# Performance work log

Hardware: AMD Instinct MI355X
Metric: run time of the kernel (lower is better)

Reference implementation:

```python
import jax, jax.numpy as jnp
import numpy as np

NUM_USERS = 600000
NUM_ITEMS = 400000
NUM_NODES = NUM_USERS + NUM_ITEMS
DIM = 64
NUM_EDGES = 8000000


def setup_inputs() -> dict:
    key = jax.random.key(0)
    k1, k2, k3, k4 = jax.random.split(key, 4)
    users_emb = jax.random.normal(k1, (NUM_USERS, DIM), dtype=jnp.float32)
    items_emb = jax.random.normal(k2, (NUM_ITEMS, DIM), dtype=jnp.float32)
    edge_index = jax.random.randint(k3, (2, NUM_EDGES), 0, NUM_NODES, dtype=jnp.int64)
    edge_values = jax.random.uniform(k4, (NUM_EDGES,), dtype=jnp.float32)
    return {
        "users_emb": users_emb,
        "items_emb": items_emb,
        "edge_index": edge_index,
        "edge_values": edge_values,
    }


def reference(users_emb, items_emb, edge_index, edge_values):
    # all_emb = cat([users_emb, items_emb])  -> [N, d]
    num_user = users_emb.shape[0]
    num_item = items_emb.shape[0]
    all_emb = jnp.concatenate([users_emb, items_emb], axis=0)
    # SpMM: out[r] = sum_{e: row[e]==r} val[e] * all_emb[col[e]]
    rows, cols = edge_index[0], edge_index[1]
    messages = all_emb[cols] * edge_values[:, None]  # [E, d] gather + scale
    out = jax.ops.segment_sum(messages, rows, num_segments=num_user + num_item)
    h_u2 = out[:num_user]
    h_i2 = out[num_user:]
    return (h_u2, h_i2)
```

## Files before the change

kernel.cpp:

```cpp
#include <hip/hip_runtime.h>

#define DIM 64
#define RPB 1024
#define RPB_SHIFT 10
#define NBMAX 1024
#define CHUNK 6144
#define EPT 24
#define CAPT 36
#define NPG 4
#define NPB 128
#define REC_CAP 1536

typedef unsigned long long u64;
typedef unsigned int u32;
typedef unsigned short u16;
typedef float f4v __attribute__((ext_vector_type(4)));
typedef _Float16 h4 __attribute__((ext_vector_type(4)));
typedef _Float16 h8 __attribute__((ext_vector_type(8)));

__global__ void detect_idx_width(const unsigned int* __restrict__ idx_words,
                                 int* __restrict__ flag) {
    __shared__ unsigned int s_or[256];
    unsigned int acc = 0;
    for (int i = threadIdx.x; i < 4096; i += blockDim.x)
        acc |= idx_words[2 * i + 1];
    s_or[threadIdx.x] = acc;
    __syncthreads();
    for (int s = 128; s > 0; s >>= 1) {
        if (threadIdx.x < s) s_or[threadIdx.x] |= s_or[threadIdx.x + s];
        __syncthreads();
    }
    if (threadIdx.x == 0) *flag = (s_or[0] == 0) ? 1 : 0;
}

__device__ __forceinline__ int load_idx(const void* ei, int use64, long long i) {
    return use64 ? (int)((const long long*)ei)[i] : ((const int*)ei)[i];
}

__device__ __forceinline__ int load_idx_nt(const void* ei, int use64, long long i) {
    return use64 ? (int)__builtin_nontemporal_load(&((const long long*)ei)[i])
                 : __builtin_nontemporal_load(&((const int*)ei)[i]);
}

__device__ __forceinline__ u32 quad_scan_ex(u32 qs, u32* wtot, int tid, u32* total_out) {
    u32 inc = qs;
    #pragma unroll
    for (int d = 1; d < 64; d <<= 1) {
        u32 v = __shfl_up(inc, d, 64);
        if ((tid & 63) >= d) inc += v;
    }
    if ((tid & 63) == 63) wtot[tid >> 6] = inc;
    __syncthreads();
    int w = tid >> 6;
    u32 woff = 0;
    #pragma unroll
    for (int k = 0; k < 3; ++k) woff += (k < w) ? wtot[k] : 0;
    if (total_out) *total_out = wtot[0] + wtot[1] + wtot[2] + wtot[3];
    return woff + inc - qs;
}

__global__ __launch_bounds__(256) void convert_emb(const f4v* __restrict__ u4,
                                                   const f4v* __restrict__ i4,
                                                   long long usz4, long long tot4,
                                                   h4* __restrict__ dst) {
    long long stride = (long long)gridDim.x * blockDim.x;
    for (long long idx = (long long)blockIdx.x * blockDim.x + threadIdx.x;
         idx < tot4; idx += stride) {
        const f4v* src = (idx < usz4) ? (u4 + idx) : (i4 + (idx - usz4));
        f4v f = __builtin_nontemporal_load(src);
        h4 o;
        o.x = (_Float16)f.x; o.y = (_Float16)f.y;
        o.z = (_Float16)f.z; o.w = (_Float16)f.w;
        dst[idx] = o;
    }
}

__global__ __launch_bounds__(256) void hist_coarse(const void* __restrict__ ei,
                                                   const int* __restrict__ flag,
                                                   int* __restrict__ counts,
                                                   int num_edges) {
    __shared__ int h[NBMAX];
    for (int b = threadIdx.x; b < NBMAX; b += 256) h[b] = 0;
    __syncthreads();
    int use64 = *flag;
    long long tid = (long long)blockIdx.x * 256 + threadIdx.x;
    long long stride = (long long)gridDim.x * 256;
    long long npairs = (long long)num_edges >> 1;
    const u64* p = (const u64*)ei;
    if (use64) {
        for (long long e = tid; e < npairs; e += stride) {
            u64 a = __builtin_nontemporal_load(&p[2 * e]);
            u64 b = __builtin_nontemporal_load(&p[2 * e + 1]);
            atomicAdd(&h[(int)(u32)a >> RPB_SHIFT], 1);
            atomicAdd(&h[(int)(u32)b >> RPB_SHIFT], 1);
        }
    } else {
        for (long long e = tid; e < npairs; e += stride) {
            u64 v = __builtin_nontemporal_load(&p[e]);
            atomicAdd(&h[(int)(u32)v >> RPB_SHIFT], 1);
            atomicAdd(&h[(int)(u32)(v >> 32) >> RPB_SHIFT], 1);
        }
    }
    if (tid == 0 && (num_edges & 1)) {
        int r = load_idx(ei, use64, num_edges - 1);
        atomicAdd(&h[r >> RPB_SHIFT], 1);
    }
    __syncthreads();
    for (int b = threadIdx.x; b < NBMAX; b += 256)
        if (h[b]) atomicAdd(&counts[b], h[b]);
}

__global__ __launch_bounds__(256) void scan_buckets(const int* __restrict__ counts,
                                                    int* __restrict__ offs,
                                                    int* __restrict__ gcursor,
                                                    int* __restrict__ offs2, int nbkt) {
    __shared__ u32 wtot[4];
    int t = threadIdx.x;
    int4 h = ((const int4*)counts)[t];
    u32 qs = (u32)(h.x + h.y + h.z + h.w);
    u32 total;
    u32 ex = quad_scan_ex(qs, wtot, t, &total);
    int o0 = (int)ex, o1 = o0 + h.x, o2 = o1 + h.y, o3 = o2 + h.z;
    offs[4*t] = o0; offs[4*t+1] = o1; offs[4*t+2] = o2; offs[4*t+3] = o3;
    gcursor[4*t] = o0; gcursor[4*t+1] = o1; gcursor[4*t+2] = o2; gcursor[4*t+3] = o3;
    if (t == 255) {
        offs[NBMAX] = (int)total;
        offs2[(long long)nbkt << RPB_SHIFT] = (int)total;
    }
}

__global__ __launch_bounds__(256, 2) void bin_edges(const void* __restrict__ ei,
                                                    const float* __restrict__ vals,
                                                    const int* __restrict__ flag,
                                                    int* __restrict__ gcursor,
                                                    u64* __restrict__ recs,
                                                    int num_edges) {
    __shared__ u32 hist[NBMAX];
    __shared__ u32 scanL[NBMAX];
    __shared__ u32 gbase[NBMAX];
    __shared__ u32 wtot[4];
    __shared__ u64 payload[CHUNK];
    __shared__ u16 bidv[CHUNK];

    int tid = threadIdx.x;
    long long base = (long long)blockIdx.x * CHUNK;
    int n = (int)min((long long)CHUNK, (long long)num_edges - base);
    int use64 = *flag;

    for (int b = tid; b < NBMAX; b += 256) hist[b] = 0;
    __syncthreads();

    int rows_[EPT]; int cols_[EPT]; float ws_[EPT];
    #pragma unroll
    for (int i = 0; i < EPT; ++i) {
        int j = tid + i * 256;
        rows_[i] = -1;
        if (j < n) {
            long long e = base + j;
            rows_[i] = load_idx_nt(ei, use64, e);
            cols_[i] = load_idx_nt(ei, use64, (long long)num_edges + e);
            ws_[i]   = __builtin_nontemporal_load(&vals[e]);
            atomicAdd(&hist[rows_[i] >> RPB_SHIFT], 1u);
        }
    }
    __syncthreads();

    u32 h0 = hist[4*tid], h1 = hist[4*tid+1], h2 = hist[4*tid+2], h3 = hist[4*tid+3];
    u32 ex = quad_scan_ex(h0 + h1 + h2 + h3, wtot, tid, nullptr);
    scanL[4*tid]   = ex;
    scanL[4*tid+1] = ex + h0;
    scanL[4*tid+2] = ex + h0 + h1;
    scanL[4*tid+3] = ex + h0 + h1 + h2;
    __syncthreads();

    for (int b = tid; b < NBMAX; b += 256) {
        u32 c = hist[b];
        gbase[b] = c ? (u32)atomicAdd(&gcursor[b], (int)c) : 0u;
    }
    __syncthreads();
    for (int b = tid; b < NBMAX; b += 256) hist[b] = scanL[b];
    __syncthreads();

    #pragma unroll
    for (int i = 0; i < EPT; ++i) {
        if (rows_[i] >= 0) {
            int b = rows_[i] >> RPB_SHIFT;
            u32 pos = atomicAdd(&hist[b], 1u);
            u32 rl = (u32)(rows_[i] & (RPB - 1));
            payload[pos] = ((u64)__float_as_uint(ws_[i]) << 32) | (rl << 20) | (u32)cols_[i];
            bidv[pos] = (u16)b;
        }
    }
    __syncthreads();

    for (int j = tid; j < n; j += 256) {
        u64 rec = payload[j];
        int b = bidv[j];
        recs[gbase[b] + (u32)j - scanL[b]] = rec;
    }
}

__global__ __launch_bounds__(256, 2) void sort_bucket(const int* __restrict__ offs,
                                                      u64* __restrict__ recs,
                                                      int* __restrict__ offs2) {
    __shared__ u32 bins[RPB];
    __shared__ u32 wtot[4];
    int b = blockIdx.x;
    int t = threadIdx.x;
    int beg = offs[b], end = offs[b + 1];
    int cnt = end - beg;
    int row0 = b << RPB_SHIFT;

    if (cnt > CAPT * 256) {
        for (int i = t; i < RPB; i += 256) offs2[row0 + i] = -(b + 1);
        return;
    }

    u64 r_[CAPT];
    #pragma unroll
    for (int k = 0; k < CAPT; ++k) {
        int j = t + k * 256;
        r_[k] = (j < cnt) ? recs[beg + j] : 0ull;
    }
    for (int i = t; i < RPB; i += 256) bins[i] = 0;
    __syncthreads();

    #pragma unroll
    for (int k = 0; k < CAPT; ++k) {
        int j = t + k * 256;
        if (j < cnt) atomicAdd(&bins[(u32)(r_[k] >> 20) & (RPB - 1)], 1u);
    }
    __syncthreads();

    u32 c0[4]; u32 s = 0;
    #pragma unroll
    for (int i = 0; i < 4; ++i) { c0[i] = bins[t * 4 + i]; s += c0[i]; }
    u32 ex = quad_scan_ex(s, wtot, t, nullptr);
    #pragma unroll
    for (int i = 0; i < 4; ++i) {
        bins[t * 4 + i] = ex;
        offs2[row0 + t * 4 + i] = beg + (int)ex;
        ex += c0[i];
    }
    __syncthreads();

    #pragma unroll
    for (int k = 0; k < CAPT; ++k) {
        int j = t + k * 256;
        if (j < cnt) {
            u32 rl = (u32)(r_[k] >> 20) & (RPB - 1);
            u32 pos = atomicAdd(&bins[rl], 1u);
            recs[beg + pos] = r_[k];
        }
    }
}

#define ACC8(P0, P1, W, V) \
    P0.x += W * (float)V[0]; P0.y += W * (float)V[1]; \
    P0.z += W * (float)V[2]; P0.w += W * (float)V[3]; \
    P1.x += W * (float)V[4]; P1.y += W * (float)V[5]; \
    P1.z += W * (float)V[6]; P1.w += W * (float)V[7];

__global__ __launch_bounds__(256) void gather_nodes_h(const int* __restrict__ offs,
                                                      const int* __restrict__ offs2,
                                                      const u64* __restrict__ recs,
                                                      const h8* __restrict__ hemb8,
                                                      float* __restrict__ out,
                                                      int num_nodes) {
    __shared__ int s_offs[NPB + 1];
    __shared__ int s_bad;
    __shared__ u64 s_recs[REC_CAP];

    int tid = threadIdx.x;
    int l8  = tid & 7;
    int g   = tid >> 3;
    long long n0 = (long long)blockIdx.x * NPB;

    if (tid == 0) s_bad = 0;
    __syncthreads();
    if (tid <= NPB) {
        int v = offs2[n0 + tid];
        s_offs[tid] = v;
        if (v < 0) s_bad = 1;
    }
    __syncthreads();

    int rbeg = s_offs[0];
    int cnt  = s_offs[NPB] - rbeg;
    bool fast = (s_bad == 0) && ((u32)cnt <= (u32)REC_CAP);

    if (fast) {
        for (int j = tid; j < cnt; j += 256)
            s_recs[j] = __builtin_nontemporal_load(&recs[rbeg + j]);
    }
    __syncthreads();

    if (fast) {
        for (int nn = 0; nn < NPG; ++nn) {
            int ln = g * NPG + nn;
            int node = (int)n0 + ln;
            if (node >= num_nodes) break;
            int beg = s_offs[ln] - rbeg;
            int end = s_offs[ln + 1] - rbeg;

            float4 p0 = make_float4(0.f,0.f,0.f,0.f), p1 = make_float4(0.f,0.f,0.f,0.f);
            float4 q0 = make_float4(0.f,0.f,0.f,0.f), q1 = make_float4(0.f,0.f,0.f,0.f);

            int i = beg;
            for (; i + 8 <= end; i += 8) {
                u64 s0 = s_recs[i];     u64 s1 = s_recs[i + 1];
                u64 s2 = s_recs[i + 2]; u64 s3 = s_recs[i + 3];
                u64 s4 = s_recs[i + 4]; u64 s5 = s_recs[i + 5];
                u64 s6 = s_recs[i + 6]; u64 s7 = s_recs[i + 7];
                h8 v0 = hemb8[(((u32)s0 & 0xFFFFFu) << 3) + l8];
                h8 v1 = hemb8[(((u32)s1 & 0xFFFFFu) << 3) + l8];
                h8 v2 = hemb8[(((u32)s2 & 0xFFFFFu) << 3) + l8];
                h8 v3 = hemb8[(((u32)s3 & 0xFFFFFu) << 3) + l8];
                h8 v4 = hemb8[(((u32)s4 & 0xFFFFFu) << 3) + l8];
                h8 v5 = hemb8[(((u32)s5 & 0xFFFFFu) << 3) + l8];
                h8 v6 = hemb8[(((u32)s6 & 0xFFFFFu) << 3) + l8];
                h8 v7 = hemb8[(((u32)s7 & 0xFFFFFu) << 3) + l8];
                float w0 = __uint_as_float((u32)(s0 >> 32));
                float w1 = __uint_as_float((u32)(s1 >> 32));
                float w2 = __uint_as_float((u32)(s2 >> 32));
                float w3 = __uint_as_float((u32)(s3 >> 32));
                float w4 = __uint_as_float((u32)(s4 >> 32));
                float w5 = __uint_as_float((u32)(s5 >> 32));
                float w6 = __uint_as_float((u32)(s6 >> 32));
                float w7 = __uint_as_float((u32)(s7 >> 32));
                ACC8(p0, p1, w0, v0); ACC8(q0, q1, w1, v1);
                ACC8(p0, p1, w2, v2); ACC8(q0, q1, w3, v3);
                ACC8(p0, p1, w4, v4); ACC8(q0, q1, w5, v5);
                ACC8(p0, p1, w6, v6); ACC8(q0, q1, w7, v7);
            }
            if (i < end) {
                int last = end - 1;
                int e1 = min(i + 1, last), e2 = min(i + 2, last);
                int e3 = min(i + 3, last), e4 = min(i + 4, last);
                int e5 = min(i + 5, last), e6 = min(i + 6, last);
                u64 s0 = s_recs[i];  u64 s1 = s_recs[e1];
                u64 s2 = s_recs[e2]; u64 s3 = s_recs[e3];
                u64 s4 = s_recs[e4]; u64 s5 = s_recs[e5];
                u64 s6 = s_recs[e6];
                h8 v0 = hemb8[(((u32)s0 & 0xFFFFFu) << 3) + l8];
                h8 v1 = hemb8[(((u32)s1 & 0xFFFFFu) << 3) + l8];
                h8 v2 = hemb8[(((u32)s2 & 0xFFFFFu) << 3) + l8];
                h8 v3 = hemb8[(((u32)s3 & 0xFFFFFu) << 3) + l8];
                h8 v4 = hemb8[(((u32)s4 & 0xFFFFFu) << 3) + l8];
                h8 v5 = hemb8[(((u32)s5 & 0xFFFFFu) << 3) + l8];
                h8 v6 = hemb8[(((u32)s6 & 0xFFFFFu) << 3) + l8];
                float w0 = __uint_as_float((u32)(s0 >> 32));
                float w1 = (i + 1 < end) ? __uint_as_float((u32)(s1 >> 32)) : 0.f;
                float w2 = (i + 2 < end) ? __uint_as_float((u32)(s2 >> 32)) : 0.f;
                float w3 = (i + 3 < end) ? __uint_as_float((u32)(s3 >> 32)) : 0.f;
                float w4 = (i + 4 < end) ? __uint_as_float((u32)(s4 >> 32)) : 0.f;
                float w5 = (i + 5 < end) ? __uint_as_float((u32)(s5 >> 32)) : 0.f;
                float w6 = (i + 6 < end) ? __uint_as_float((u32)(s6 >> 32)) : 0.f;
                ACC8(p0, p1, w0, v0); ACC8(q0, q1, w1, v1);
                ACC8(p0, p1, w2, v2); ACC8(q0, q1, w3, v3);
                ACC8(p0, p1, w4, v4); ACC8(q0, q1, w5, v5);
                ACC8(p0, p1, w6, v6);
            }

            p0.x += q0.x; p0.y += q0.y; p0.z += q0.z; p0.w += q0.w;
            p1.x += q1.x; p1.y += q1.y; p1.z += q1.z; p1.w += q1.w;
            f4v o0; o0.x = p0.x; o0.y = p0.y; o0.z = p0.z; o0.w = p0.w;
            f4v o1; o1.x = p1.x; o1.y = p1.y; o1.z = p1.z; o1.w = p1.w;
            f4v* dst = (f4v*)out + ((long long)node << 4) + (l8 << 1);
            __builtin_nontemporal_store(o0, dst);
            __builtin_nontemporal_store(o1, dst + 1);
        }
    } else {
        for (int nn = 0; nn < NPG; ++nn) {
            int ln = g * NPG + nn;
            int node = (int)n0 + ln;
            if (node >= num_nodes) break;
            int beg = s_offs[ln];
            int end = s_offs[ln + 1];
            if (beg < 0) { int b = node >> RPB_SHIFT; beg = offs[b]; end = offs[b + 1]; }
            else if (end < 0) { end = offs[(node >> RPB_SHIFT) + 1]; }
            u32 rl = (u32)(node & (RPB - 1));

            float4 p0 = make_float4(0.f,0.f,0.f,0.f), p1 = make_float4(0.f,0.f,0.f,0.f);
            float4 q0 = make_float4(0.f,0.f,0.f,0.f), q1 = make_float4(0.f,0.f,0.f,0.f);
            int last = end - 1;
            u32 rm = RPB - 1;
            for (int i = beg; i < end; i += 4) {
                int e1 = min(i + 1, last), e2 = min(i + 2, last), e3 = min(i + 3, last);
                u64 s0 = recs[i];  u64 s1 = recs[e1];
                u64 s2 = recs[e2]; u64 s3 = recs[e3];
                h8 v0 = hemb8[(((u32)s0 & 0xFFFFFu) << 3) + l8];
                h8 v1 = hemb8[(((u32)s1 & 0xFFFFFu) << 3) + l8];
                h8 v2 = hemb8[(((u32)s2 & 0xFFFFFu) << 3) + l8];
                h8 v3 = hemb8[(((u32)s3 & 0xFFFFFu) << 3) + l8];
                float w0 = ((((u32)(s0 >> 20)) & rm) == rl)
                           ? __uint_as_float((u32)(s0 >> 32)) : 0.f;
                float w1 = (((((u32)(s1 >> 20)) & rm) == rl) & (i + 1 < end))
                           ? __uint_as_float((u32)(s1 >> 32)) : 0.f;
                float w2 = (((((u32)(s2 >> 20)) & rm) == rl) & (i + 2 < end))
                           ? __uint_as_float((u32)(s2 >> 32)) : 0.f;
                float w3 = (((((u32)(s3 >> 20)) & rm) == rl) & (i + 3 < end))
                           ? __uint_as_float((u32)(s3 >> 32)) : 0.f;
                ACC8(p0, p1, w0, v0); ACC8(q0, q1, w1, v1);
                ACC8(p0, p1, w2, v2); ACC8(q0, q1, w3, v3);
            }
            p0.x += q0.x; p0.y += q0.y; p0.z += q0.z; p0.w += q0.w;
            p1.x += q1.x; p1.y += q1.y; p1.z += q1.z; p1.w += q1.w;
            f4v o0; o0.x = p0.x; o0.y = p0.y; o0.z = p0.z; o0.w = p0.w;
            f4v o1; o1.x = p1.x; o1.y = p1.y; o1.z = p1.z; o1.w = p1.w;
            f4v* dst = (f4v*)out + ((long long)node << 4) + (l8 << 1);
            __builtin_nontemporal_store(o0, dst);
            __builtin_nontemporal_store(o1, dst + 1);
        }
    }
}

__device__ __forceinline__ void gstep(u64 s, u32 rl,
                                      const float* __restrict__ users,
                                      const float* __restrict__ items_m,
                                      int num_users, int l16, float4& a) {
    int c = (int)(s & 0xFFFFFu);
    float w = __uint_as_float((u32)(s >> 32));
    w = (((u32)(s >> 20) & (RPB - 1)) == rl) ? w : 0.f;
    const float* p = ((c < num_users) ? users : items_m) + ((u32)c << 6);
    float4 m = reinterpret_cast<const float4*>(p)[l16];
    a.x += w * m.x; a.y += w * m.y; a.z += w * m.z; a.w += w * m.w;
}

__global__ __launch_bounds__(256) void gather_nodes(const int* __restrict__ offs,
                                                    const int* __restrict__ offs2,
                                                    const u64* __restrict__ recs,
                                                    const float* __restrict__ users,
                                                    const float* __restrict__ items_m,
                                                    float* __restrict__ out,
                                                    int num_users, int num_nodes) {
    int node = blockIdx.x * (blockDim.x >> 6) + (threadIdx.x >> 6);
    int lane = threadIdx.x & 63;
    if (node >= num_nodes) return;
    int q   = lane >> 4;
    int l16 = lane & 15;

    int beg = offs2[node];
    int end = offs2[node + 1];
    if (beg < 0) { int b = node >> RPB_SHIFT; beg = offs[b]; end = offs[b + 1]; }
    else if (end < 0) { end = offs[(node >> RPB_SHIFT) + 1]; }
    u32 rl = (u32)(node & (RPB - 1));

    float4 a0 = make_float4(0.f, 0.f, 0.f, 0.f);
    float4 a1 = make_float4(0.f, 0.f, 0.f, 0.f);

    int i = beg + q;
    for (; i + 4 < end; i += 8) {
        u64 s0 = recs[i];
        u64 s1 = recs[i + 4];
        gstep(s0, rl, users, items_m, num_users, l16, a0);
        gstep(s1, rl, users, items_m, num_users, l16, a1);
    }
    if (i < end) {
        u64 s0 = recs[i];
        gstep(s0, rl, users, items_m, num_users, l16, a0);
    }
    a0.x += a1.x; a0.y += a1.y; a0.z += a1.z; a0.w += a1.w;

    for (int msk = 16; msk <= 32; msk <<= 1) {
        a0.x += __shfl_xor(a0.x, msk, 64);
        a0.y += __shfl_xor(a0.y, msk, 64);
        a0.z += __shfl_xor(a0.z, msk, 64);
        a0.w += __shfl_xor(a0.w, msk, 64);
    }
    if (q == 0)
        reinterpret_cast<float4*>(out)[(long long)node * 16 + l16] = a0;
}

__global__ __launch_bounds__(256) void scatter_edges(const void* __restrict__ edge_index,
                                                     const float* __restrict__ vals,
                                                     const float* __restrict__ users,
                                                     const float* __restrict__ items,
                                                     float* __restrict__ out,
                                                     const int* __restrict__ idx64_flag,
                                                     int num_users, int num_edges) {
    long long gid = (long long)blockIdx.x * blockDim.x + threadIdx.x;
    long long e = gid >> 4;
    int lane = (int)(gid & 15);
    if (e >= num_edges) return;
    int use64 = *idx64_flag;
    int r = load_idx(edge_index, use64, e);
    int c = load_idx(edge_index, use64, (long long)num_edges + e);
    float w = vals[e];
    const float* src = (c < num_users)
        ? (users + (long long)c * DIM)
        : (items + (long long)(c - num_users) * DIM);
    float4 m = reinterpret_cast<const float4*>(src)[lane];
    float* dst = out + (long long)r * DIM + lane * 4;
    unsafeAtomicAdd(dst + 0, m.x * w);
    unsafeAtomicAdd(dst + 1, m.y * w);
    unsafeAtomicAdd(dst + 2, m.z * w);
    unsafeAtomicAdd(dst + 3, m.w * w);
}

extern "C" void kernel_launch(void* const* d_in, const int* in_sizes, int n_in,
                              void* d_out, int out_size, void* d_ws, size_t ws_size,
                              hipStream_t stream) {
    const float* users = (const float*)d_in[0];
    const float* items = (const float*)d_in[1];
    const void*  eidx  = d_in[2];
    const float* vals  = (const float*)d_in[3];
    float* out = (float*)d_out;

    int num_users = in_sizes[0] / DIM;
    int num_items = in_sizes[1] / DIM;
    int num_nodes = num_users + num_items;
    int num_edges = in_sizes[3];
    int nbkt = (num_nodes + RPB - 1) >> RPB_SHIFT;

    size_t off = 0;
    auto alloc = [&](size_t bytes) { size_t p = off; off = (off + bytes + 255) & ~(size_t)255; return p; };
    size_t o_flag   = alloc(4);
    size_t o_counts = alloc((size_t)NBMAX * 4);
    size_t o_offs   = alloc(((size_t)NBMAX + 1) * 4);
    size_t o_gcur   = alloc((size_t)NBMAX * 4);
    size_t o_recs   = alloc((size_t)num_edges * 8 + 64);
    size_t o_offs2  = alloc((((size_t)nbkt << RPB_SHIFT) + 1) * 4);
    size_t need_base = off;
    size_t o_hemb   = alloc((size_t)num_nodes * DIM * 2);
    size_t need_f16 = off;

    char* ws = (char*)d_ws;
    int* flag = (int*)(ws + o_flag);

    detect_idx_width<<<1, 256, 0, stream>>>((const unsigned int*)eidx, flag);

    if (ws_size < need_base || nbkt > NBMAX || num_nodes > (1 << 20)) {
        hipMemsetAsync(d_out, 0, (size_t)out_size * sizeof(float), stream);
        long long total_threads = (long long)num_edges * 16;
        long long grid = (total_threads + 255) / 256;
        scatter_edges<<<(int)grid, 256, 0, stream>>>(
            eidx, vals, users, items, out, flag, num_users, num_edges);
        return;
    }

    int* counts  = (int*)(ws + o_counts);
    int* offs    = (int*)(ws + o_offs);
    int* gcursor = (int*)(ws + o_gcur);
    u64* recs    = (u64*)(ws + o_recs);
    int* offs2   = (int*)(ws + o_offs2);
    h4*  hemb4   = (h4*)(ws + o_hemb);

    bool use_f16 = (ws_size >= need_f16) && ((DIM % 8) == 0);

    hipMemsetAsync(counts, 0, (size_t)NBMAX * 4, stream);

    if (use_f16) {
        long long usz4 = (long long)num_users * DIM / 4;
        long long tot4 = (long long)num_nodes * DIM / 4;
        convert_emb<<<2048, 256, 0, stream>>>((const f4v*)users, (const f4v*)items,
                                              usz4, tot4, hemb4);
    }

    hist_coarse<<<768, 256, 0, stream>>>(eidx, flag, counts, num_edges);
    scan_buckets<<<1, 256, 0, stream>>>(counts, offs, gcursor, offs2, nbkt);

    int bin_grid = (num_edges + CHUNK - 1) / CHUNK;
    bin_edges<<<bin_grid, 256, 0, stream>>>(eidx, vals, flag, gcursor, recs, num_edges);

    sort_bucket<<<nbkt, 256, 0, stream>>>(offs, recs, offs2);

    if (use_f16) {
        int gg = (num_nodes + NPB - 1) / NPB;
        gather_nodes_h<<<gg, 256, 0, stream>>>(offs, offs2, recs,
                                               (const h8*)hemb4, out, num_nodes);
    } else {
        int gg = (num_nodes + 3) / 4;
        const float* items_m = items - (size_t)num_users * DIM;
        gather_nodes<<<gg, 256, 0, stream>>>(offs, offs2, recs, users, items_m, out,
                                             num_users, num_nodes);
    }
}
```

Baseline: 473.1 us.

## Fuse per-bucket counting sort into f16 gather kernel using shared-memory records

The separate sort_bucket and gather_nodes_h kernels on the f16 path are merged into one kernel, sortgather_h, with one block per 1024-row bucket. Each block loads the bucket's records into registers, counting-sorts them into LDS, and then gathers directly from shared memory. This removes the sorted-record write-back to global memory, the re-read, and the offs2 array, at the cost of large LDS use (about 70KB per block) and only 1024-row granularity parallelism. Bin chunk size and EPT are also reduced, and the occupancy hint is dropped from bin_edges.

New measurement: 399.6 us. -15.5%, faster.

```diff
diff --git a/kernel.cpp b/kernel.cpp
--- a/kernel.cpp
+++ b/kernel.cpp
@@ -4,12 +4,11 @@
 #define RPB 1024
 #define RPB_SHIFT 10
 #define NBMAX 1024
-#define CHUNK 6144
-#define EPT 24
-#define CAPT 36
-#define NPG 4
-#define NPB 128
-#define REC_CAP 1536
+#define CHUNK 4096
+#define EPT 16
+#define CAPT 35
+#define SREC_CAP (CAPT * 256)
+#define NPGF 32
 
 typedef unsigned long long u64;
 typedef unsigned int u32;
@@ -125,16 +124,16 @@
     gcursor[4*t] = o0; gcursor[4*t+1] = o1; gcursor[4*t+2] = o2; gcursor[4*t+3] = o3;
     if (t == 255) {
         offs[NBMAX] = (int)total;
-        offs2[(long long)nbkt << RPB_SHIFT] = (int)total;
-    }
-}
-
-__global__ __launch_bounds__(256, 2) void bin_edges(const void* __restrict__ ei,
-                                                    const float* __restrict__ vals,
-                                                    const int* __restrict__ flag,
-                                                    int* __restrict__ gcursor,
-                                                    u64* __restrict__ recs,
-                                                    int num_edges) {
+        if (offs2) offs2[(long long)nbkt << RPB_SHIFT] = (int)total;
+    }
+}
+
+__global__ __launch_bounds__(256) void bin_edges(const void* __restrict__ ei,
+                                                 const float* __restrict__ vals,
+                                                 const int* __restrict__ flag,
+                                                 int* __restrict__ gcursor,
+                                                 u64* __restrict__ recs,
+                                                 int num_edges) {
     __shared__ u32 hist[NBMAX];
     __shared__ u32 scanL[NBMAX];
     __shared__ u32 gbase[NBMAX];
@@ -200,114 +199,80 @@
     }
 }
 
-__global__ __launch_bounds__(256, 2) void sort_bucket(const int* __restrict__ offs,
-                                                      u64* __restrict__ recs,
-                                                      int* __restrict__ offs2) {
-    __shared__ u32 bins[RPB];
-    __shared__ u32 wtot[4];
-    int b = blockIdx.x;
-    int t = threadIdx.x;
-    int beg = offs[b], end = offs[b + 1];
-    int cnt = end - beg;
-    int row0 = b << RPB_SHIFT;
-
-    if (cnt > CAPT * 256) {
-        for (int i = t; i < RPB; i += 256) offs2[row0 + i] = -(b + 1);
-        return;
-    }
-
-    u64 r_[CAPT];
-    #pragma unroll
-    for (int k = 0; k < CAPT; ++k) {
-        int j = t + k * 256;
-        r_[k] = (j < cnt) ? recs[beg + j] : 0ull;
-    }
-    for (int i = t; i < RPB; i += 256) bins[i] = 0;
-    __syncthreads();
-
-    #pragma unroll
-    for (int k = 0; k < CAPT; ++k) {
-        int j = t + k * 256;
-        if (j < cnt) atomicAdd(&bins[(u32)(r_[k] >> 20) & (RPB - 1)], 1u);
-    }
-    __syncthreads();
-
-    u32 c0[4]; u32 s = 0;
-    #pragma unroll
-    for (int i = 0; i < 4; ++i) { c0[i] = bins[t * 4 + i]; s += c0[i]; }
-    u32 ex = quad_scan_ex(s, wtot, t, nullptr);
-    #pragma unroll
-    for (int i = 0; i < 4; ++i) {
-        bins[t * 4 + i] = ex;
-        offs2[row0 + t * 4 + i] = beg + (int)ex;
-        ex += c0[i];
-    }
-    __syncthreads();
-
-    #pragma unroll
-    for (int k = 0; k < CAPT; ++k) {
-        int j = t + k * 256;
-        if (j < cnt) {
-            u32 rl = (u32)(r_[k] >> 20) & (RPB - 1);
-            u32 pos = atomicAdd(&bins[rl], 1u);
-            recs[beg + pos] = r_[k];
-        }
-    }
-}
-
 #define ACC8(P0, P1, W, V) \
     P0.x += W * (float)V[0]; P0.y += W * (float)V[1]; \
     P0.z += W * (float)V[2]; P0.w += W * (float)V[3]; \
     P1.x += W * (float)V[4]; P1.y += W * (float)V[5]; \
     P1.z += W * (float)V[6]; P1.w += W * (float)V[7];
 
-__global__ __launch_bounds__(256) void gather_nodes_h(const int* __restrict__ offs,
-                                                      const int* __restrict__ offs2,
-                                                      const u64* __restrict__ recs,
-                                                      const h8* __restrict__ hemb8,
-                                                      float* __restrict__ out,
-                                                      int num_nodes) {
-    __shared__ int s_offs[NPB + 1];
-    __shared__ int s_bad;
-    __shared__ u64 s_recs[REC_CAP];
-
-    int tid = threadIdx.x;
-    int l8  = tid & 7;
-    int g   = tid >> 3;
-    long long n0 = (long long)blockIdx.x * NPB;
-
-    if (tid == 0) s_bad = 0;
-    __syncthreads();
-    if (tid <= NPB) {
-        int v = offs2[n0 + tid];
-        s_offs[tid] = v;
-        if (v < 0) s_bad = 1;
-    }
-    __syncthreads();
-
-    int rbeg = s_offs[0];
-    int cnt  = s_offs[NPB] - rbeg;
-    bool fast = (s_bad == 0) && ((u32)cnt <= (u32)REC_CAP);
-
-    if (fast) {
-        for (int j = tid; j < cnt; j += 256)
-            s_recs[j] = __builtin_nontemporal_load(&recs[rbeg + j]);
-    }
-    __syncthreads();
-
-    if (fast) {
-        for (int nn = 0; nn < NPG; ++nn) {
-            int ln = g * NPG + nn;
-            int node = (int)n0 + ln;
+__global__ __launch_bounds__(256, 2) void sortgather_h(const int* __restrict__ offs,
+                                                       const u64* __restrict__ recs,
+                                                       const h8* __restrict__ hemb8,
+                                                       float* __restrict__ out,
+                                                       int num_nodes) {
+    __shared__ u64 s_recs[SREC_CAP];
+    __shared__ u32 node_beg[RPB + 1];
+    __shared__ u32 cursor[RPB];
+    __shared__ u32 wtot[4];
+
+    int b  = blockIdx.x;
+    int t  = threadIdx.x;
+    int l8 = t & 7;
+    int g  = t >> 3;
+    int beg = offs[b], end = offs[b + 1];
+    int cnt = end - beg;
+    int row0 = b << RPB_SHIFT;
+
+    if (cnt <= SREC_CAP) {
+        u64 r_[CAPT];
+        #pragma unroll
+        for (int k = 0; k < CAPT; ++k) {
+            int j = t + k * 256;
+            r_[k] = (j < cnt) ? __builtin_nontemporal_load(&recs[beg + j]) : 0ull;
+        }
+        for (int i = t; i < RPB; i += 256) cursor[i] = 0;
+        __syncthreads();
+        #pragma unroll
+        for (int k = 0; k < CAPT; ++k) {
+            int j = t + k * 256;
+            if (j < cnt) atomicAdd(&cursor[(u32)(r_[k] >> 20) & (RPB - 1)], 1u);
+        }
+        __syncthreads();
+        u32 c0[4]; u32 s = 0;
+        #pragma unroll
+        for (int i = 0; i < 4; ++i) { c0[i] = cursor[t * 4 + i]; s += c0[i]; }
+        u32 ex = quad_scan_ex(s, wtot, t, nullptr);
+        #pragma unroll
+        for (int i = 0; i < 4; ++i) {
+            node_beg[t * 4 + i] = ex;
+            cursor[t * 4 + i] = ex;
+            ex += c0[i];
+        }
+        if (t == 0) node_beg[RPB] = (u32)cnt;
+        __syncthreads();
+        #pragma unroll
+        for (int k = 0; k < CAPT; ++k) {
+            int j = t + k * 256;
+            if (j < cnt) {
+                u32 rl = (u32)(r_[k] >> 20) & (RPB - 1);
+                u32 pos = atomicAdd(&cursor[rl], 1u);
+                s_recs[pos] = r_[k];
+            }
+        }
+        __syncthreads();
+
+        for (int nn = 0; nn < NPGF; ++nn) {
+            int ln = g * NPGF + nn;
+            int node = row0 + ln;
             if (node >= num_nodes) break;
-            int beg = s_offs[ln] - rbeg;
-            int end = s_offs[ln + 1] - rbeg;
+            int nb = (int)node_beg[ln];
+            int ne = (int)node_beg[ln + 1];
 
             float4 p0 = make_float4(0.f,0.f,0.f,0.f), p1 = make_float4(0.f,0.f,0.f,0.f);
             float4 q0 = make_float4(0.f,0.f,0.f,0.f), q1 = make_float4(0.f,0.f,0.f,0.f);
 
-            int i = beg;
-            for (; i + 8 <= end; i += 8) {
+            int i = nb;
+            for (; i + 8 <= ne; i += 8) {
                 u64 s0 = s_recs[i];     u64 s1 = s_recs[i + 1];
                 u64 s2 = s_recs[i + 2]; u64 s3 = s_recs[i + 3];
                 u64 s4 = s_recs[i + 4]; u64 s5 = s_recs[i + 5];
@@ -333,8 +298,8 @@
                 ACC8(p0, p1, w4, v4); ACC8(q0, q1, w5, v5);
                 ACC8(p0, p1, w6, v6); ACC8(q0, q1, w7, v7);
             }
-            if (i < end) {
-                int last = end - 1;
+            if (i < ne) {
+                int last = ne - 1;
                 int e1 = min(i + 1, last), e2 = min(i + 2, last);
                 int e3 = min(i + 3, last), e4 = min(i + 4, last);
                 int e5 = min(i + 5, last), e6 = min(i + 6, last);
@@ -350,12 +315,12 @@
                 h8 v5 = hemb8[(((u32)s5 & 0xFFFFFu) << 3) + l8];
                 h8 v6 = hemb8[(((u32)s6 & 0xFFFFFu) << 3) + l8];
                 float w0 = __uint_as_float((u32)(s0 >> 32));
-                float w1 = (i + 1 < end) ? __uint_as_float((u32)(s1 >> 32)) : 0.f;
-                float w2 = (i + 2 < end) ? __uint_as_float((u32)(s2 >> 32)) : 0.f;
-                float w3 = (i + 3 < end) ? __uint_as_float((u32)(s3 >> 32)) : 0.f;
-                float w4 = (i + 4 < end) ? __uint_as_float((u32)(s4 >> 32)) : 0.f;
-                float w5 = (i + 5 < end) ? __uint_as_float((u32)(s5 >> 32)) : 0.f;
-                float w6 = (i + 6 < end) ? __uint_as_float((u32)(s6 >> 32)) : 0.f;
+                float w1 = (i + 1 < ne) ? __uint_as_float((u32)(s1 >> 32)) : 0.f;
+                float w2 = (i + 2 < ne) ? __uint_as_float((u32)(s2 >> 32)) : 0.f;
+                float w3 = (i + 3 < ne) ? __uint_as_float((u32)(s3 >> 32)) : 0.f;
+                float w4 = (i + 4 < ne) ? __uint_as_float((u32)(s4 >> 32)) : 0.f;
+                float w5 = (i + 5 < ne) ? __uint_as_float((u32)(s5 >> 32)) : 0.f;
+                float w6 = (i + 6 < ne) ? __uint_as_float((u32)(s6 >> 32)) : 0.f;
                 ACC8(p0, p1, w0, v0); ACC8(q0, q1, w1, v1);
                 ACC8(p0, p1, w2, v2); ACC8(q0, q1, w3, v3);
                 ACC8(p0, p1, w4, v4); ACC8(q0, q1, w5, v5);
@@ -371,15 +336,11 @@
             __builtin_nontemporal_store(o1, dst + 1);
         }
     } else {
-        for (int nn = 0; nn < NPG; ++nn) {
-            int ln = g * NPG + nn;
-            int node = (int)n0 + ln;
+        for (int nn = 0; nn < NPGF; ++nn) {
+            int ln = g * NPGF + nn;
+            int node = row0 + ln;
             if (node >= num_nodes) break;
-            int beg = s_offs[ln];
-            int end = s_offs[ln + 1];
-            if (beg < 0) { int b = node >> RPB_SHIFT; beg = offs[b]; end = offs[b + 1]; }
-            else if (end < 0) { end = offs[(node >> RPB_SHIFT) + 1]; }
-            u32 rl = (u32)(node & (RPB - 1));
+            u32 rl = (u32)ln;
 
             float4 p0 = make_float4(0.f,0.f,0.f,0.f), p1 = make_float4(0.f,0.f,0.f,0.f);
             float4 q0 = make_float4(0.f,0.f,0.f,0.f), q1 = make_float4(0.f,0.f,0.f,0.f);
@@ -415,6 +376,61 @@
     }
 }
 
+__global__ __launch_bounds__(256, 2) void sort_bucket(const int* __restrict__ offs,
+                                                      u64* __restrict__ recs,
+                                                      int* __restrict__ offs2) {
+    __shared__ u32 bins[RPB];
+    __shared__ u32 wtot[4];
+    int b = blockIdx.x;
+    int t = threadIdx.x;
+    int beg = offs[b], end = offs[b + 1];
+    int cnt = end - beg;
+    int row0 = b << RPB_SHIFT;
+
+    if (cnt > CAPT * 256) {
+        for (int i = t; i < RPB; i += 256) offs2[row0 + i] = -(b + 1);
+        return;
+    }
+
+    u64 r_[CAPT];
+    #pragma unroll
+    for (int k = 0; k < CAPT; ++k) {
+        int j = t + k * 256;
+        r_[k] = (j < cnt) ? recs[beg + j] : 0ull;
+    }
+    for (int i = t; i < RPB; i += 256) bins[i] = 0;
+    __syncthreads();
+
+    #pragma unroll
+    for (int k = 0; k < CAPT; ++k) {
+        int j = t + k * 256;
+        if (j < cnt) atomicAdd(&bins[(u32)(r_[k] >> 20) & (RPB - 1)], 1u);
+    }
+    __syncthreads();
+
+    u32 c0[4]; u32 s = 0;
+    #pragma unroll
+    for (int i = 0; i < 4; ++i) { c0[i] = bins[t * 4 + i]; s += c0[i]; }
+    u32 ex = quad_scan_ex(s, wtot, t, nullptr);
+    #pragma unroll
+    for (int i = 0; i < 4; ++i) {
+        bins[t * 4 + i] = ex;
+        offs2[row0 + t * 4 + i] = beg + (int)ex;
+        ex += c0[i];
+    }
+    __syncthreads();
+
+    #pragma unroll
+    for (int k = 0; k < CAPT; ++k) {
+        int j = t + k * 256;
+        if (j < cnt) {
+            u32 rl = (u32)(r_[k] >> 20) & (RPB - 1);
+            u32 pos = atomicAdd(&bins[rl], 1u);
+            recs[beg + pos] = r_[k];
+        }
+    }
+}
+
 __device__ __forceinline__ void gstep(u64 s, u32 rl,
                                       const float* __restrict__ users,
                                       const float* __restrict__ items_m,
@@ -558,18 +574,17 @@
     }
 
     hist_coarse<<<768, 256, 0, stream>>>(eidx, flag, counts, num_edges);
-    scan_buckets<<<1, 256, 0, stream>>>(counts, offs, gcursor, offs2, nbkt);
+    scan_buckets<<<1, 256, 0, stream>>>(counts, offs, gcursor,
+                                        use_f16 ? nullptr : offs2, nbkt);
 
     int bin_grid = (num_edges + CHUNK - 1) / CHUNK;
     bin_edges<<<bin_grid, 256, 0, stream>>>(eidx, vals, flag, gcursor, recs, num_edges);
 
-    sort_bucket<<<nbkt, 256, 0, stream>>>(offs, recs, offs2);
-
     if (use_f16) {
-        int gg = (num_nodes + NPB - 1) / NPB;
-        gather_nodes_h<<<gg, 256, 0, stream>>>(offs, offs2, recs,
-                                               (const h8*)hemb4, out, num_nodes);
+        sortgather_h<<<nbkt, 256, 0, stream>>>(offs, recs, (const h8*)hemb4,
+                                               out, num_nodes);
     } else {
+        sort_bucket<<<nbkt, 256, 0, stream>>>(offs, recs, offs2);
         int gg = (num_nodes + 3) / 4;
         const float* items_m = items - (size_t)num_users * DIM;
         gather_nodes<<<gg, 256, 0, stream>>>(offs, offs2, recs, users, items_m, out,
```
